# Performance work log

Measured on AMD Instinct MI355X. Metric: run time of the kernel, lower is better.

## Reference

```python
import jax, jax.numpy as jnp
import numpy as np

WIN = 7            # skimage default win_size
NP_ = WIN * WIN    # pixels per 2D window (per channel)
COV_NORM = NP_ / (NP_ - 1.0)  # use_sample_covariance=True
K1, K2 = 0.01, 0.03


def setup_inputs() -> dict:
    key = jax.random.key(0)
    k1, k2 = jax.random.split(key)
    img1 = jax.random.uniform(k1, (32, 3, 512, 512), dtype=jnp.float32)
    img2 = jax.random.uniform(k2, (32, 3, 512, 512), dtype=jnp.float32)
    return {"img1": img1, "img2": img2}


def _uf(x):
    # valid 7x7 uniform (mean) filter; x: [N, 1, H, W] -> [N, 1, H-6, W-6]
    # independent of boundary mode.
    k = jnp.ones((1, 1, WIN, WIN), x.dtype) / NP_
    return jax.lax.conv_general_dilated(
        x, k, window_strides=(1, 1), padding='VALID',
        dimension_numbers=('NCHW', 'OIHW', 'NCHW'))


def reference(img1, img2):
    B, C, H, W = img1.shape
    x = img1.reshape(B * C, 1, H, W)
    y = img2.reshape(B * C, 1, H, W)

    ux, uy = _uf(x), _uf(y)
    uxx, uyy, uxy = _uf(x * x), _uf(y * y), _uf(x * y)
    vx = COV_NORM * (uxx - ux * ux)
    vy = COV_NORM * (uyy - uy * uy)
    vxy = COV_NORM * (uxy - ux * uy)

    # per-image data_range = img2[i].max() - img2[i].min() (over C,H,W)
    dr = jnp.max(img2, axis=(1, 2, 3)) - jnp.min(img2, axis=(1, 2, 3))  # [B]
    dr = jnp.repeat(dr, C).reshape(B * C, 1, 1, 1)
    C1 = (K1 * dr) ** 2
    C2 = (K2 * dr) ** 2

    S = ((2.0 * ux * uy + C1) * (2.0 * vxy + C2)) / \
        ((ux * ux + uy * uy + C1) * (vx + vy + C2))

    # skimage: mean over cropped map per channel, mean over channels, then batch mean
    ssim_per_img = S.reshape(B, C, H - WIN + 1, W - WIN + 1).mean(axis=(1, 2, 3))
    return 1.0 - ssim_per_img.mean()
```

## Files before the change

### kernel.cpp

```cpp
#include <hip/hip_runtime.h>

#define IMG_H 512
#define IMG_W 512
#define NIMG 96
#define WOUT 506
#define STRIP 11
#define NSTRIPS 46
#define NBLK (NSTRIPS*NIMG)
#define TOTAL_VALS 24579456.0f

#define WS_MN 0
#define WS_MX 8192
#define WS_SS 16384
#define WS_NEED ((WS_SS + NBLK) * 4)

__device__ __forceinline__ int swz(int bid){
    return (bid & 7) * (NBLK / 8) + (bid >> 3);
}

__global__ __launch_bounds__(64) void minmax_part(const float* __restrict__ img2,
                                                  float* __restrict__ ws){
    int L     = swz(blockIdx.x);
    int img   = L / NSTRIPS;
    int strip = L - img * NSTRIPS;
    int r0    = strip * STRIP;

    const float4* y4 = (const float4*)(img2 + (size_t)img * (IMG_H*IMG_W)) + r0 * 128;
    float mn = 3.4e38f, mx = -3.4e38f;
    #pragma unroll 4
    for (int i = threadIdx.x; i < 17*128; i += 64){
        float4 v = y4[i];
        mn = fminf(mn, fminf(fminf(v.x, v.y), fminf(v.z, v.w)));
        mx = fmaxf(mx, fmaxf(fmaxf(v.x, v.y), fmaxf(v.z, v.w)));
    }
    #pragma unroll
    for (int off = 32; off; off >>= 1){
        mn = fminf(mn, __shfl_down(mn, off));
        mx = fmaxf(mx, __shfl_down(mx, off));
    }
    if (threadIdx.x == 0){
        ws[WS_MN + L] = mn;
        ws[WS_MX + L] = mx;
    }
}


#define ROWOP(row, OPA) { \
    const float* xr = x + (size_t)(row)*IMG_W + c0; \
    const float* yr = y + (size_t)(row)*IMG_W + c0; \
    float4 xa = *(const float4*)xr;     float4 xb = *(const float4*)(xr+4); \
    float4 ya = *(const float4*)yr;     float4 yb = *(const float4*)(yr+4); \
    float xv[8] = {xa.x,xa.y,xa.z,xa.w,xb.x,xb.y,xb.z,xb.w}; \
    float yv[8] = {ya.x,ya.y,ya.z,ya.w,yb.x,yb.y,yb.z,yb.w}; \
    _Pragma("unroll") \
    for (int k = 0; k < 8; k++){ \
        sx[k]  OPA xv[k]; \
        sy[k]  OPA yv[k]; \
        sxx[k] OPA xv[k]*xv[k]; \
        syy[k] OPA yv[k]*yv[k]; \
        sxy[k] OPA xv[k]*yv[k]; \
    } }

#define HSHUF(s, outw) { \
    float n0=__shfl_down(s[0],1), n1=__shfl_down(s[1],1), n2=__shfl_down(s[2],1); \
    float n3=__shfl_down(s[3],1), n4=__shfl_down(s[4],1), n5=__shfl_down(s[5],1); \
    float w = s[0]+s[1]+s[2]+s[3]+s[4]+s[5]+s[6]; \
    outw[0]=w; \
    w += s[7]-s[0]; outw[1]=w; \
    w += n0-s[1];   outw[2]=w; \
    w += n1-s[2];   outw[3]=w; \
    w += n2-s[3];   outw[4]=w; \
    w += n3-s[4];   outw[5]=w; \
    w += n4-s[5];   outw[6]=w; \
    w += n5-s[6];   outw[7]=w; }

template<int USE_WS>
__global__ __launch_bounds__(64) void ssim_kernel(const float* __restrict__ img1,
                                                  const float* __restrict__ img2,
                                                  float* __restrict__ ws,
                                                  float* __restrict__ acc){
    int L     = swz(blockIdx.x);
    int img   = L / NSTRIPS;
    int strip = L - img * NSTRIPS;
    int b     = img / 3;

    float mn = 3.4e38f, mx = -3.4e38f;
    if (USE_WS){
        const float* pmn = ws + WS_MN + b * 3 * NSTRIPS;
        const float* pmx = ws + WS_MX + b * 3 * NSTRIPS;
        #pragma unroll 6
        for (int i = 0; i < 3*NSTRIPS; i++){
            mn = fminf(mn, pmn[i]);
            mx = fmaxf(mx, pmx[i]);
        }
    } else {
        unsigned mk = ((const unsigned*)ws)[b];
        unsigned nk = ((const unsigned*)ws)[32 + b];
        unsigned mb = (mk & 0x80000000u) ? (mk ^ 0x80000000u) : ~mk;
        unsigned nb = (nk & 0x80000000u) ? (nk ^ 0x80000000u) : ~nk;
        mx = __uint_as_float(mb); mn = __uint_as_float(nb);
    }
    float dr = mx - mn;
    float c1 = 0.01f * dr;  c1 *= c1;
    float c2 = 0.03f * dr;  c2 *= c2;
    const float c1s = 2401.0f * c1;
    const float c2s = 2401.0f * c2;
    const float CO2 = 2.0f * 49.0f / 48.0f;
    const float COV = 49.0f / 48.0f;

    const float* x = img1 + (size_t)img * (IMG_H*IMG_W);
    const float* y = img2 + (size_t)img * (IMG_H*IMG_W);

    int t  = threadIdx.x;
    int c0 = t * 8;

    float sx[8]={0,0,0,0,0,0,0,0}, sy[8]={0,0,0,0,0,0,0,0};
    float sxx[8]={0,0,0,0,0,0,0,0}, syy[8]={0,0,0,0,0,0,0,0}, sxy[8]={0,0,0,0,0,0,0,0};

    int r0 = strip * STRIP;

    #pragma unroll
    for (int rr = 0; rr < 7; rr++){ ROWOP(r0+rr, +=) }

    float accS = 0.0f;

    for (int r = r0; r < r0 + STRIP; r++){
        bool more = (r < r0 + STRIP - 1);
        float4 EX0,EX1,EY0,EY1, LX0,LX1,LY0,LY1;
        if (more){
            const float* xe = x + (size_t)(r+7)*IMG_W + c0;
            const float* ye = y + (size_t)(r+7)*IMG_W + c0;
            const float* xl = x + (size_t)r*IMG_W + c0;
            const float* yl = y + (size_t)r*IMG_W + c0;
            EX0 = *(const float4*)xe;  EX1 = *(const float4*)(xe+4);
            EY0 = *(const float4*)ye;  EY1 = *(const float4*)(ye+4);
            LX0 = *(const float4*)xl;  LX1 = *(const float4*)(xl+4);
            LY0 = *(const float4*)yl;  LY1 = *(const float4*)(yl+4);
        }

        float wsx[8], wsy[8], wsxx[8], wsyy[8], wsxy[8];
        HSHUF(sx, wsx)  HSHUF(sy, wsy)  HSHUF(sxx, wsxx)
        HSHUF(syy, wsyy)  HSHUF(sxy, wsxy)

        #pragma unroll
        for (int j = 0; j < 8; j++){
            if (c0 + j < WOUT){
                float P = wsx[j], Q = wsy[j];
                float t1 = P*Q;
                float t2 = fmaf(P, P, Q*Q);
                float a1 = fmaf(2.0f, t1, c1s);
                float b1 = t2 + c1s;
                float u  = fmaf(49.0f, wsxy[j], -t1);
                float a2 = fmaf(CO2, u, c2s);
                float v  = fmaf(49.0f, wsxx[j]+wsyy[j], -t2);
                float b2 = fmaf(COV, v, c2s);
                accS += (a1*a2) * __builtin_amdgcn_rcpf(b1*b2);
            }
        }

        if (more){
            float xv[8] = {EX0.x,EX0.y,EX0.z,EX0.w,EX1.x,EX1.y,EX1.z,EX1.w};
            float yv[8] = {EY0.x,EY0.y,EY0.z,EY0.w,EY1.x,EY1.y,EY1.z,EY1.w};
            float lx[8] = {LX0.x,LX0.y,LX0.z,LX0.w,LX1.x,LX1.y,LX1.z,LX1.w};
            float ly[8] = {LY0.x,LY0.y,LY0.z,LY0.w,LY1.x,LY1.y,LY1.z,LY1.w};
            #pragma unroll
            for (int k = 0; k < 8; k++){
                sx[k]  += xv[k] - lx[k];
                sy[k]  += yv[k] - ly[k];
                sxx[k] += xv[k]*xv[k] - lx[k]*lx[k];
                syy[k] += yv[k]*yv[k] - ly[k]*ly[k];
                sxy[k] += xv[k]*yv[k] - lx[k]*ly[k];
            }
        }
    }

    #pragma unroll
    for (int off = 32; off; off >>= 1)
        accS += __shfl_down(accS, off);
    if (t == 0){
        if (USE_WS) ws[WS_SS + L] = accS;
        else        atomicAdd(acc, accS);
    }
}

__global__ __launch_bounds__(64) void finalize_ws(const float* __restrict__ ws,
                                                  float* __restrict__ out){
    float s = 0.0f;
    for (int i = threadIdx.x; i < NBLK; i += 64) s += ws[WS_SS + i];
    #pragma unroll
    for (int off = 32; off; off >>= 1) s += __shfl_down(s, off);
    if (threadIdx.x == 0) out[0] = 1.0f - s * (1.0f / TOTAL_VALS);
}

__global__ void finalize_acc(const float* __restrict__ acc, float* __restrict__ out){
    out[0] = 1.0f - acc[0] * (1.0f / TOTAL_VALS);
}

__device__ __forceinline__ unsigned fkey(float f){
    unsigned b = __float_as_uint(f);
    return (b & 0x80000000u) ? ~b : (b | 0x80000000u);
}
__global__ __launch_bounds__(256) void minmax_atomic(const float4* __restrict__ y4,
                                                     unsigned* __restrict__ ws){
    int blk  = blockIdx.x;
    int img  = blk >> 6;
    int chnk = blk & 63;
    const float4* base = y4 + (size_t)img * 196608 + (size_t)chnk * 3072;
    float mn = 3.4e38f, mx = -3.4e38f;
    for (int i = threadIdx.x; i < 3072; i += 256){
        float4 v = base[i];
        mn = fminf(mn, fminf(fminf(v.x, v.y), fminf(v.z, v.w)));
        mx = fmaxf(mx, fmaxf(fmaxf(v.x, v.y), fmaxf(v.z, v.w)));
    }
    #pragma unroll
    for (int off = 32; off; off >>= 1){
        mn = fminf(mn, __shfl_down(mn, off));
        mx = fmaxf(mx, __shfl_down(mx, off));
    }
    if ((threadIdx.x & 63) == 0){
        atomicMax(&ws[img], fkey(mx));
        atomicMin(&ws[32 + img], fkey(mn));
    }
}

extern "C" void kernel_launch(void* const* d_in, const int* in_sizes, int n_in,
                              void* d_out, int out_size, void* d_ws, size_t ws_size,
                              hipStream_t stream) {
    const float* img1 = (const float*)d_in[0];
    const float* img2 = (const float*)d_in[1];
    float* out = (float*)d_out;
    float* ws  = (float*)d_ws;

    if (ws_size >= WS_NEED){
        minmax_part<<<NBLK, 64, 0, stream>>>(img2, ws);
        ssim_kernel<1><<<NBLK, 64, 0, stream>>>(img1, img2, ws, nullptr);
        finalize_ws<<<1, 64, 0, stream>>>(ws, out);
    } else {
        hipMemsetAsync(ws, 0, 160, stream);
        hipMemsetAsync((char*)ws + 128, 0xFF, 128, stream);
        hipMemsetAsync((char*)ws + 256, 0, 16, stream);
        float* acc = ws + 64;
        minmax_atomic<<<2048, 256, 0, stream>>>((const float4*)img2, (unsigned*)ws);
        ssim_kernel<0><<<NBLK, 64, 0, stream>>>(img1, img2, ws, acc);
        finalize_acc<<<1, 1, 0, stream>>>(acc, out);
    }
}
```

Baseline: 287.5 us.

## Software-pipeline row loads in SSIM kernel, stream window math, and rechunk min/max pass

The SSIM strip loop is fully unrolled, and the next incoming row is prefetched one iteration ahead so global-load latency overlaps the window computation. The horizontal 7-tap sums are now advanced in a running fashion and consumed immediately instead of being stored into five 8-wide arrays, and the vertical update uses FMAs. The min/max pre-pass switches from 4416 blocks of 64 threads, which also reread overlapping rows, to 1536 blocks of 256 threads over disjoint 16K-element chunks. This cuts redundant reads and the number of partials each SSIM block has to reduce, at the cost of higher register pressure from the prefetch, with launch bounds raised to request 4 blocks per CU.

Result: slower. 374.8 us (+30.3%).

```diff
diff --git a/kernel.cpp b/kernel.cpp
--- a/kernel.cpp
+++ b/kernel.cpp
@@ -8,6 +8,7 @@
 #define NSTRIPS 46
 #define NBLK (NSTRIPS*NIMG)
 #define TOTAL_VALS 24579456.0f
+#define MM_CHUNKS 16
 
 #define WS_MN 0
 #define WS_MX 8192
@@ -18,18 +19,17 @@
     return (bid & 7) * (NBLK / 8) + (bid >> 3);
 }
 
-__global__ __launch_bounds__(64) void minmax_part(const float* __restrict__ img2,
-                                                  float* __restrict__ ws){
-    int L     = swz(blockIdx.x);
-    int img   = L / NSTRIPS;
-    int strip = L - img * NSTRIPS;
-    int r0    = strip * STRIP;
-
-    const float4* y4 = (const float4*)(img2 + (size_t)img * (IMG_H*IMG_W)) + r0 * 128;
+__global__ __launch_bounds__(256) void minmax_part(const float* __restrict__ img2,
+                                                   float* __restrict__ ws){
+    __shared__ float s_mn[4], s_mx[4];
+    int blk  = blockIdx.x;
+    int img  = blk >> 4;
+    int chnk = blk & 15;
+    const float4* base = (const float4*)(img2 + (size_t)img * (IMG_H*IMG_W)) + chnk * 4096;
     float mn = 3.4e38f, mx = -3.4e38f;
     #pragma unroll 4
-    for (int i = threadIdx.x; i < 17*128; i += 64){
-        float4 v = y4[i];
+    for (int i = threadIdx.x; i < 4096; i += 256){
+        float4 v = base[i];
         mn = fminf(mn, fminf(fminf(v.x, v.y), fminf(v.z, v.w)));
         mx = fmaxf(mx, fmaxf(fmaxf(v.x, v.y), fmaxf(v.z, v.w)));
     }
@@ -38,9 +38,14 @@
         mn = fminf(mn, __shfl_down(mn, off));
         mx = fmaxf(mx, __shfl_down(mx, off));
     }
+    int wave = threadIdx.x >> 6;
+    if ((threadIdx.x & 63) == 0){ s_mn[wave] = mn; s_mx[wave] = mx; }
+    __syncthreads();
     if (threadIdx.x == 0){
-        ws[WS_MN + L] = mn;
-        ws[WS_MX + L] = mx;
+        mn = fminf(fminf(s_mn[0], s_mn[1]), fminf(s_mn[2], s_mn[3]));
+        mx = fmaxf(fmaxf(s_mx[0], s_mx[1]), fmaxf(s_mx[2], s_mx[3]));
+        ws[WS_MN + blk] = mn;
+        ws[WS_MX + blk] = mx;
     }
 }
 
@@ -61,24 +66,29 @@
         sxy[k] OPA xv[k]*yv[k]; \
     } }
 
-#define HSHUF(s, outw) { \
-    float n0=__shfl_down(s[0],1), n1=__shfl_down(s[1],1), n2=__shfl_down(s[2],1); \
-    float n3=__shfl_down(s[3],1), n4=__shfl_down(s[4],1), n5=__shfl_down(s[5],1); \
-    float w = s[0]+s[1]+s[2]+s[3]+s[4]+s[5]+s[6]; \
-    outw[0]=w; \
-    w += s[7]-s[0]; outw[1]=w; \
-    w += n0-s[1];   outw[2]=w; \
-    w += n1-s[2];   outw[3]=w; \
-    w += n2-s[3];   outw[4]=w; \
-    w += n3-s[4];   outw[5]=w; \
-    w += n4-s[5];   outw[6]=w; \
-    w += n5-s[6];   outw[7]=w; }
+#define SSIMJ(j) { \
+    if (c0 + (j) < WOUT){ \
+        float P_ = wx, Q_ = wy; \
+        float t1_ = P_*Q_; \
+        float t2_ = fmaf(P_, P_, Q_*Q_); \
+        float a1_ = fmaf(2.0f, t1_, c1s); \
+        float b1_ = t2_ + c1s; \
+        float u_  = fmaf(49.0f, wxy, -t1_); \
+        float a2_ = fmaf(CO2, u_, c2s); \
+        float v_  = fmaf(49.0f, wxx+wyy, -t2_); \
+        float b2_ = fmaf(COV, v_, c2s); \
+        accS += (a1_*a2_) * __builtin_amdgcn_rcpf(b1_*b2_); \
+    } }
+
+#define WADV(ax,bx, ay,by, axx,bxx, ayy,byy, axy,bxy) \
+    wx  += (ax)  - (bx);   wy  += (ay)  - (by); \
+    wxx += (axx) - (bxx);  wyy += (ayy) - (byy);  wxy += (axy) - (bxy);
 
 template<int USE_WS>
-__global__ __launch_bounds__(64) void ssim_kernel(const float* __restrict__ img1,
-                                                  const float* __restrict__ img2,
-                                                  float* __restrict__ ws,
-                                                  float* __restrict__ acc){
+__global__ __launch_bounds__(64, 4) void ssim_kernel(const float* __restrict__ img1,
+                                                     const float* __restrict__ img2,
+                                                     float* __restrict__ ws,
+                                                     float* __restrict__ acc){
     int L     = swz(blockIdx.x);
     int img   = L / NSTRIPS;
     int strip = L - img * NSTRIPS;
@@ -86,10 +96,10 @@
 
     float mn = 3.4e38f, mx = -3.4e38f;
     if (USE_WS){
-        const float* pmn = ws + WS_MN + b * 3 * NSTRIPS;
-        const float* pmx = ws + WS_MX + b * 3 * NSTRIPS;
-        #pragma unroll 6
-        for (int i = 0; i < 3*NSTRIPS; i++){
+        const float* pmn = ws + WS_MN + b * 3 * MM_CHUNKS;
+        const float* pmx = ws + WS_MX + b * 3 * MM_CHUNKS;
+        #pragma unroll 8
+        for (int i = 0; i < 3*MM_CHUNKS; i++){
             mn = fminf(mn, pmn[i]);
             mx = fmaxf(mx, pmx[i]);
         }
@@ -113,65 +123,80 @@
 
     int t  = threadIdx.x;
     int c0 = t * 8;
+    int r0 = strip * STRIP;
 
     float sx[8]={0,0,0,0,0,0,0,0}, sy[8]={0,0,0,0,0,0,0,0};
     float sxx[8]={0,0,0,0,0,0,0,0}, syy[8]={0,0,0,0,0,0,0,0}, sxy[8]={0,0,0,0,0,0,0,0};
 
-    int r0 = strip * STRIP;
-
     #pragma unroll
     for (int rr = 0; rr < 7; rr++){ ROWOP(r0+rr, +=) }
 
+    float4 eX0, eX1, eY0, eY1;
+    {
+        const float* xe = x + (size_t)(r0+7)*IMG_W + c0;
+        const float* ye = y + (size_t)(r0+7)*IMG_W + c0;
+        eX0 = *(const float4*)xe;  eX1 = *(const float4*)(xe+4);
+        eY0 = *(const float4*)ye;  eY1 = *(const float4*)(ye+4);
+    }
+
     float accS = 0.0f;
 
-    for (int r = r0; r < r0 + STRIP; r++){
-        bool more = (r < r0 + STRIP - 1);
-        float4 EX0,EX1,EY0,EY1, LX0,LX1,LY0,LY1;
-        if (more){
-            const float* xe = x + (size_t)(r+7)*IMG_W + c0;
-            const float* ye = y + (size_t)(r+7)*IMG_W + c0;
-            const float* xl = x + (size_t)r*IMG_W + c0;
-            const float* yl = y + (size_t)r*IMG_W + c0;
-            EX0 = *(const float4*)xe;  EX1 = *(const float4*)(xe+4);
-            EY0 = *(const float4*)ye;  EY1 = *(const float4*)(ye+4);
-            LX0 = *(const float4*)xl;  LX1 = *(const float4*)(xl+4);
-            LY0 = *(const float4*)yl;  LY1 = *(const float4*)(yl+4);
-        }
-
-        float wsx[8], wsy[8], wsxx[8], wsyy[8], wsxy[8];
-        HSHUF(sx, wsx)  HSHUF(sy, wsy)  HSHUF(sxx, wsxx)
-        HSHUF(syy, wsyy)  HSHUF(sxy, wsxy)
-
-        #pragma unroll
-        for (int j = 0; j < 8; j++){
-            if (c0 + j < WOUT){
-                float P = wsx[j], Q = wsy[j];
-                float t1 = P*Q;
-                float t2 = fmaf(P, P, Q*Q);
-                float a1 = fmaf(2.0f, t1, c1s);
-                float b1 = t2 + c1s;
-                float u  = fmaf(49.0f, wsxy[j], -t1);
-                float a2 = fmaf(CO2, u, c2s);
-                float v  = fmaf(49.0f, wsxx[j]+wsyy[j], -t2);
-                float b2 = fmaf(COV, v, c2s);
-                accS += (a1*a2) * __builtin_amdgcn_rcpf(b1*b2);
-            }
-        }
-
-        if (more){
-            float xv[8] = {EX0.x,EX0.y,EX0.z,EX0.w,EX1.x,EX1.y,EX1.z,EX1.w};
-            float yv[8] = {EY0.x,EY0.y,EY0.z,EY0.w,EY1.x,EY1.y,EY1.z,EY1.w};
-            float lx[8] = {LX0.x,LX0.y,LX0.z,LX0.w,LX1.x,LX1.y,LX1.z,LX1.w};
-            float ly[8] = {LY0.x,LY0.y,LY0.z,LY0.w,LY1.x,LY1.y,LY1.z,LY1.w};
+    #pragma unroll
+    for (int i = 0; i < STRIP; i++){
+        float4 nX0, nX1, nY0, nY1, lX0, lX1, lY0, lY1;
+        if (i < STRIP-2){
+            const float* xe = x + (size_t)(r0+8+i)*IMG_W + c0;
+            const float* ye = y + (size_t)(r0+8+i)*IMG_W + c0;
+            nX0 = *(const float4*)xe;  nX1 = *(const float4*)(xe+4);
+            nY0 = *(const float4*)ye;  nY1 = *(const float4*)(ye+4);
+        }
+        if (i < STRIP-1){
+            const float* xl = x + (size_t)(r0+i)*IMG_W + c0;
+            const float* yl = y + (size_t)(r0+i)*IMG_W + c0;
+            lX0 = *(const float4*)xl;  lX1 = *(const float4*)(xl+4);
+            lY0 = *(const float4*)yl;  lY1 = *(const float4*)(yl+4);
+        }
+
+        float nx0=__shfl_down(sx[0],1),  nx1=__shfl_down(sx[1],1),  nx2=__shfl_down(sx[2],1),
+              nx3=__shfl_down(sx[3],1),  nx4=__shfl_down(sx[4],1),  nx5=__shfl_down(sx[5],1);
+        float ny0=__shfl_down(sy[0],1),  ny1=__shfl_down(sy[1],1),  ny2=__shfl_down(sy[2],1),
+              ny3=__shfl_down(sy[3],1),  ny4=__shfl_down(sy[4],1),  ny5=__shfl_down(sy[5],1);
+        float nxx0=__shfl_down(sxx[0],1), nxx1=__shfl_down(sxx[1],1), nxx2=__shfl_down(sxx[2],1),
+              nxx3=__shfl_down(sxx[3],1), nxx4=__shfl_down(sxx[4],1), nxx5=__shfl_down(sxx[5],1);
+        float nyy0=__shfl_down(syy[0],1), nyy1=__shfl_down(syy[1],1), nyy2=__shfl_down(syy[2],1),
+              nyy3=__shfl_down(syy[3],1), nyy4=__shfl_down(syy[4],1), nyy5=__shfl_down(syy[5],1);
+        float nxy0=__shfl_down(sxy[0],1), nxy1=__shfl_down(sxy[1],1), nxy2=__shfl_down(sxy[2],1),
+              nxy3=__shfl_down(sxy[3],1), nxy4=__shfl_down(sxy[4],1), nxy5=__shfl_down(sxy[5],1);
+
+        float wx  = sx[0]+sx[1]+sx[2]+sx[3]+sx[4]+sx[5]+sx[6];
+        float wy  = sy[0]+sy[1]+sy[2]+sy[3]+sy[4]+sy[5]+sy[6];
+        float wxx = sxx[0]+sxx[1]+sxx[2]+sxx[3]+sxx[4]+sxx[5]+sxx[6];
+        float wyy = syy[0]+syy[1]+syy[2]+syy[3]+syy[4]+syy[5]+syy[6];
+        float wxy = sxy[0]+sxy[1]+sxy[2]+sxy[3]+sxy[4]+sxy[5]+sxy[6];
+        SSIMJ(0)
+        WADV(sx[7],sx[0], sy[7],sy[0], sxx[7],sxx[0], syy[7],syy[0], sxy[7],sxy[0])  SSIMJ(1)
+        WADV(nx0,sx[1],  ny0,sy[1],  nxx0,sxx[1],  nyy0,syy[1],  nxy0,sxy[1])        SSIMJ(2)
+        WADV(nx1,sx[2],  ny1,sy[2],  nxx1,sxx[2],  nyy1,syy[2],  nxy1,sxy[2])        SSIMJ(3)
+        WADV(nx2,sx[3],  ny2,sy[3],  nxx2,sxx[3],  nyy2,syy[3],  nxy2,sxy[3])        SSIMJ(4)
+        WADV(nx3,sx[4],  ny3,sy[4],  nxx3,sxx[4],  nyy3,syy[4],  nxy3,sxy[4])        SSIMJ(5)
+        WADV(nx4,sx[5],  ny4,sy[5],  nxx4,sxx[5],  nyy4,syy[5],  nxy4,sxy[5])        SSIMJ(6)
+        WADV(nx5,sx[6],  ny5,sy[6],  nxx5,sxx[6],  nyy5,syy[6],  nxy5,sxy[6])        SSIMJ(7)
+
+        if (i < STRIP-1){
+            float xv[8]  = {eX0.x,eX0.y,eX0.z,eX0.w, eX1.x,eX1.y,eX1.z,eX1.w};
+            float yv[8]  = {eY0.x,eY0.y,eY0.z,eY0.w, eY1.x,eY1.y,eY1.z,eY1.w};
+            float lxv[8] = {lX0.x,lX0.y,lX0.z,lX0.w, lX1.x,lX1.y,lX1.z,lX1.w};
+            float lyv[8] = {lY0.x,lY0.y,lY0.z,lY0.w, lY1.x,lY1.y,lY1.z,lY1.w};
             #pragma unroll
             for (int k = 0; k < 8; k++){
-                sx[k]  += xv[k] - lx[k];
-                sy[k]  += yv[k] - ly[k];
-                sxx[k] += xv[k]*xv[k] - lx[k]*lx[k];
-                syy[k] += yv[k]*yv[k] - ly[k]*ly[k];
-                sxy[k] += xv[k]*yv[k] - lx[k]*ly[k];
+                sx[k]  += xv[k] - lxv[k];
+                sy[k]  += yv[k] - lyv[k];
+                sxx[k] = fmaf(xv[k], xv[k], fmaf(-lxv[k], lxv[k], sxx[k]));
+                syy[k] = fmaf(yv[k], yv[k], fmaf(-lyv[k], lyv[k], syy[k]));
+                sxy[k] = fmaf(xv[k], yv[k], fmaf(-lxv[k], lyv[k], sxy[k]));
             }
         }
+        if (i < STRIP-2){ eX0=nX0; eX1=nX1; eY0=nY0; eY1=nY1; }
     }
 
     #pragma unroll
@@ -232,7 +257,7 @@
     float* ws  = (float*)d_ws;
 
     if (ws_size >= WS_NEED){
-        minmax_part<<<NBLK, 64, 0, stream>>>(img2, ws);
+        minmax_part<<<NIMG*MM_CHUNKS, 256, 0, stream>>>(img2, ws);
         ssim_kernel<1><<<NBLK, 64, 0, stream>>>(img1, img2, ws, nullptr);
         finalize_ws<<<1, 64, 0, stream>>>(ws, out);
     } else {
```
